# Performance work log

Measured on AMD Instinct MI355X. Metric: run time of the kernel, lower is better.

The kernel has to match this reference:

```python
import jax, jax.numpy as jnp
import numpy as np

EPS = 1e-8
TAU = 0.2
IOU_THR = 0.5
NEG = -1e9
N, C, H, D_FG, D_CLS = 8192, 1024, 256, 64, 128


def setup_inputs() -> dict:
    key = jax.random.key(0)
    ks = jax.random.split(key, 11)
    def lin(k, fan_in, fan_out):
        return jax.random.normal(k, (fan_in, fan_out), jnp.float32) / np.sqrt(fan_in)
    return {
        "roi_feats": jax.random.normal(ks[0], (N, C), jnp.float32),
        "labels": jax.random.randint(ks[1], (N,), 0, 21, jnp.int32).astype(jnp.int64),
        "ious": jax.random.uniform(ks[2], (N,), jnp.float32),
        "fg_w1": lin(ks[3], C, H), "fg_b1": jnp.zeros((H,), jnp.float32),
        "fg_w2": lin(ks[4], H, D_FG), "fg_b2": jnp.zeros((D_FG,), jnp.float32),
        "cls_w1": lin(ks[5], C, H), "cls_b1": jnp.zeros((H,), jnp.float32),
        "cls_w2": lin(ks[6], H, D_CLS), "cls_b2": jnp.zeros((D_CLS,), jnp.float32),
    }


def _project_normalize(x, w1, b1, w2, b2):
    h = jax.nn.relu(x @ w1 + b1)
    z = h @ w2 + b2
    norm = jnp.maximum(jnp.linalg.norm(z, axis=1, keepdims=True), EPS)
    return z / norm


def _forward(roi_feats, labels, ious, fg_w1, fg_b1, fg_w2, fg_b2, cls_w1, cls_b1, cls_w2, cls_b2):
    n = roi_feats.shape[0]
    z_fg = _project_normalize(roi_feats, fg_w1, fg_b1, fg_w2, fg_b2)
    z_cls = _project_normalize(roi_feats, cls_w1, cls_b1, cls_w2, cls_b2)

    ignore = labels == -1
    fg = (labels > 0) & ~ignore
    iou_weight = jnp.where(ious > IOU_THR, ious, 0.0)
    eye = jnp.eye(n, dtype=bool)

    # ---- fg/bg contrastive (bg_as_negatives_only=True) ----
    sim_fg = (z_fg @ z_fg.T) / TAU                       # [N,N]
    exp_sim = jnp.exp(sim_fg)
    denom = jnp.sum(exp_sim * (~eye).astype(jnp.float32), axis=1)
    pos = (fg & ~ignore)[None, :] & ~eye                 # positives: fg columns, no self
    n_pos = jnp.sum(pos, axis=1)
    numer = jnp.sum(exp_sim * pos.astype(jnp.float32), axis=1)
    # original computes den = denom + EPS then -log((numer+EPS)/(den+EPS))
    loss_i = -jnp.log((numer + EPS) / (denom + 2.0 * EPS))
    valid = (fg & ~ignore) & (n_pos > 0)
    w = iou_weight * valid.astype(jnp.float32)
    loss_fg_bg = jnp.sum(w * loss_i) / (jnp.sum(w) + EPS)

    # ---- class supervised contrastive ----
    sim_cls = (z_cls @ z_cls.T) / TAU
    sim_masked = jnp.where(eye, NEG, sim_cls)
    log_denom = jax.nn.logsumexp(sim_masked, axis=1)     # [N]
    log_p = jnp.where(eye, NEG, sim_cls - log_denom[:, None])
    # pos_mask keeps diagonal (as in original): same label, col not ignore, col label != 0
    posc = (labels[None, :] == labels[:, None]) & (~ignore)[None, :] & (labels[None, :] != 0)
    n_posc = jnp.sum(posc, axis=1).astype(jnp.float32)
    sum_log_p = jnp.sum(log_p * posc.astype(jnp.float32), axis=1)
    valid_c = (fg & ~ignore) & (n_posc > 0) & jnp.isfinite(log_denom)
    Lzi = jnp.where(valid_c, -sum_log_p / (n_posc + EPS), 0.0)
    wc = iou_weight * valid_c.astype(jnp.float32)
    loss_supcon = jnp.sum(wc * Lzi) / (jnp.sum(wc) + EPS)

    return jnp.stack([loss_fg_bg, loss_supcon])


def reference(roi_feats, labels, ious, fg_w1, fg_b1, fg_w2, fg_b2, cls_w1, cls_b1, cls_w2, cls_b2):
    return _forward(roi_feats, labels, ious, fg_w1, fg_b1, fg_w2, fg_b2, cls_w1, cls_b1, cls_w2, cls_b2)
```

## Files before the change

### kernel.cpp

```cpp
#include <hip/hip_runtime.h>


typedef __attribute__((ext_vector_type(8))) short bs8;
typedef __attribute__((ext_vector_type(4))) float f4;

#define MFMA_BF16(a, b, c) __builtin_amdgcn_mfma_f32_16x16x32_bf16((a), (b), (c), 0, 0, 0)
#define EXP2F(x) exp2f(x)
#define SQRT_KL2E 2.6857914f
#define LN2F      0.6931471805599453f

__device__ __forceinline__ unsigned short f2bf(float f) {
  unsigned int u = __float_as_uint(f);
  u = (u + 0x7fffu + ((u >> 16) & 1u)) >> 16;
  return (unsigned short)u;
}
__device__ __forceinline__ float bf2f(unsigned short s) {
  return __uint_as_float(((unsigned int)s) << 16);
}
__device__ __forceinline__ unsigned int pk_trunc(float a, float b) {
  return __builtin_amdgcn_perm(__float_as_uint(b), __float_as_uint(a), 0x07060302u);
}

constexpr size_t O_W1T  = 0;
constexpr size_t O_W2TF = 1048576;
constexpr size_t O_W2TC = 1081344;
constexpr size_t O_SCLS = 1146880;
constexpr size_t O_ROWD = 1163264;
constexpr size_t O_ROWN = 1196032;
constexpr size_t O_ROWS = 1228800;
constexpr size_t O_SCAL = 1261568;
constexpr size_t O_HIST = 1261584;
constexpr size_t O_NFG  = 1261712;
constexpr size_t O_H    = 1261824;
constexpr size_t O_ZF   = 9650432;
constexpr size_t O_ZC   = 10699008;
constexpr size_t O_XB   = 12796160;
constexpr size_t WS_NEED_XB = O_XB + 16777216;
constexpr int ZERO_WORDS = (int)((O_SCAL + 16 - O_SCLS) / 4);

__global__ void __launch_bounds__(256) prep_kernel(
    const float* __restrict__ X, const int* __restrict__ labels,
    const float* __restrict__ fgw1, const float* __restrict__ clsw1,
    const float* __restrict__ fgw2, const float* __restrict__ clsw2,
    unsigned short* __restrict__ W1T, unsigned short* __restrict__ W2Tf,
    unsigned short* __restrict__ W2Tc, float* __restrict__ zerop,
    int* __restrict__ hist, int* __restrict__ nfg,
    unsigned short* __restrict__ Xb) {
  const int bx = blockIdx.x, t = threadIdx.x;
  if (bx < 113) {
    int i = bx * 256 + t;
    if (i < ZERO_WORDS) zerop[i] = 0.f;
    return;
  }
  if (bx == 113) {
    __shared__ int sh[33];
    if (t < 33) sh[t] = 0;
    __syncthreads();
    for (int it = 0; it < 32; it++) {
      int lab = labels[it * 256 + t];
      if (lab >= 0 && lab < 32) atomicAdd(&sh[lab], 1);
      if (lab > 0) atomicAdd(&sh[32], 1);
    }
    __syncthreads();
    if (t < 32) hist[t] = sh[t];
    if (t == 32) *nfg = sh[32];
    return;
  }
  if (bx < 254) {
    __shared__ float tile[64][65];
    int lb = bx - 114;
    const float* src; unsigned short* dst; int R, C, lt;
    if (lb < 64)       { src = fgw1;  dst = W1T;              R = 1024; C = 256; lt = lb; }
    else if (lb < 128) { src = clsw1; dst = W1T + 256 * 1024; R = 1024; C = 256; lt = lb - 64; }
    else if (lb < 132) { src = fgw2;  dst = W2Tf;             R = 256;  C = 64;  lt = lb - 128; }
    else               { src = clsw2; dst = W2Tc;             R = 256;  C = 128; lt = lb - 132; }
    const int cT = C >> 6;
    const int r0 = (lt / cT) << 6, c0 = (lt % cT) << 6;
    {
      const int rr = t >> 4, cc = (t & 15) << 2;
#pragma unroll
      for (int i = 0; i < 4; i++) {
        float4 v = *(const float4*)(src + (size_t)(r0 + rr + i * 16) * C + c0 + cc);
        tile[rr + i * 16][cc] = v.x; tile[rr + i * 16][cc + 1] = v.y;
        tile[rr + i * 16][cc + 2] = v.z; tile[rr + i * 16][cc + 3] = v.w;
      }
    }
    __syncthreads();
    {
      const int dr = t >> 2, dc = (t & 3) << 4;
      bs8 o0, o1;
#pragma unroll
      for (int j = 0; j < 8; j++) o0[j] = (short)f2bf(tile[dc + j][dr]);
#pragma unroll
      for (int j = 0; j < 8; j++) o1[j] = (short)f2bf(tile[dc + 8 + j][dr]);
      unsigned short* dp = dst + (size_t)(c0 + dr) * R + r0 + dc;
      *(bs8*)dp = o0;
      *(bs8*)(dp + 8) = o1;
    }
    return;
  }
  {
    int i = (bx - 254) * 2048 + t * 8;
    float4 x0 = *(const float4*)(X + i);
    float4 x1 = *(const float4*)(X + i + 4);
    uint4 pk;
    pk.x = pk_trunc(x0.x, x0.y);
    pk.y = pk_trunc(x0.z, x0.w);
    pk.z = pk_trunc(x1.x, x1.y);
    pk.w = pk_trunc(x1.z, x1.w);
    *(uint4*)(Xb + i) = pk;
  }
}

__global__ void __launch_bounds__(256) gemm1x_kernel(
    const unsigned short* __restrict__ Xb, const unsigned short* __restrict__ W1T,
    const float* __restrict__ b1f, const float* __restrict__ b1c,
    unsigned short* __restrict__ H) {
  __shared__ __align__(16) unsigned short lA[128 * 72];
  __shared__ __align__(16) unsigned short lB[64 * 72];
  const int t = threadIdx.x;
  const int w = t >> 6, lane = t & 63, ln = lane & 15, quad = lane >> 4;
  const int m0 = blockIdx.x * 128, n0 = blockIdx.y * 64;

  f4 acc[2][4];
#pragma unroll
  for (int rs = 0; rs < 2; rs++)
#pragma unroll
    for (int s = 0; s < 4; s++) acc[rs][s] = (f4){0.f, 0.f, 0.f, 0.f};

  for (int k0 = 0; k0 < 1024; k0 += 64) {
    __syncthreads();
#pragma unroll
    for (int i = 0; i < 4; i++) {
      int c = i * 256 + t, r = c >> 3, ke = (c & 7) * 8;
      *(bs8*)&lA[r * 72 + ke] = *(const bs8*)(Xb + (size_t)(m0 + r) * 1024 + k0 + ke);
    }
#pragma unroll
    for (int i = 0; i < 2; i++) {
      int c = i * 256 + t, r = c >> 3, ke = (c & 7) * 8;
      *(bs8*)&lB[r * 72 + ke] = *(const bs8*)(W1T + (size_t)(n0 + r) * 1024 + k0 + ke);
    }
    __syncthreads();
#pragma unroll
    for (int kk = 0; kk < 2; kk++) {
      bs8 a0 = *(const bs8*)&lA[(w * 32 + ln) * 72 + kk * 32 + quad * 8];
      bs8 a1 = *(const bs8*)&lA[(w * 32 + 16 + ln) * 72 + kk * 32 + quad * 8];
#pragma unroll
      for (int s = 0; s < 4; s++) {
        bs8 bf = *(const bs8*)&lB[(s * 16 + ln) * 72 + kk * 32 + quad * 8];
        acc[0][s] = MFMA_BF16(a0, bf, acc[0][s]);
        acc[1][s] = MFMA_BF16(a1, bf, acc[1][s]);
      }
    }
  }
#pragma unroll
  for (int s = 0; s < 4; s++) {
    int n = n0 + s * 16 + ln;
    float b = (n < 256) ? b1f[n] : b1c[n - 256];
#pragma unroll
    for (int rs = 0; rs < 2; rs++)
#pragma unroll
      for (int r = 0; r < 4; r++) {
        float v = fmaxf(acc[rs][s][r] + b, 0.f);
        H[(size_t)(m0 + w * 32 + rs * 16 + quad * 4 + r) * 512 + n] = f2bf(v);
      }
  }
}

__global__ void __launch_bounds__(256) gemm1f_kernel(
    const float* __restrict__ X, const unsigned short* __restrict__ W1T,
    const float* __restrict__ b1f, const float* __restrict__ b1c,
    unsigned short* __restrict__ H) {
  __shared__ __align__(16) unsigned short lA[128 * 40];
  __shared__ __align__(16) unsigned short lB[64 * 40];
  const int t = threadIdx.x;
  const int w = t >> 6, lane = t & 63, ln = lane & 15, quad = lane >> 4;
  const int m0 = blockIdx.x * 128, n0 = blockIdx.y * 64;
  f4 acc[2][4];
#pragma unroll
  for (int rs = 0; rs < 2; rs++)
#pragma unroll
    for (int s = 0; s < 4; s++) acc[rs][s] = (f4){0.f, 0.f, 0.f, 0.f};
  for (int k0 = 0; k0 < 1024; k0 += 32) {
    __syncthreads();
#pragma unroll
    for (int i = 0; i < 2; i++) {
      int ch = t + i * 256;
      int r = ch >> 2, c = (ch & 3) * 8;
      const float* xp = X + (size_t)(m0 + r) * 1024 + k0 + c;
      float4 x0 = *(const float4*)xp;
      float4 x1 = *(const float4*)(xp + 4);
      uint4 pk;
      pk.x = pk_trunc(x0.x, x0.y); pk.y = pk_trunc(x0.z, x0.w);
      pk.z = pk_trunc(x1.x, x1.y); pk.w = pk_trunc(x1.z, x1.w);
      *(uint4*)&lA[r * 40 + c] = pk;
    }
    {
      int r = t >> 2, c = (t & 3) * 8;
      *(bs8*)&lB[r * 40 + c] = *(const bs8*)(W1T + (size_t)(n0 + r) * 1024 + k0 + c);
    }
    __syncthreads();
    bs8 af0 = *(const bs8*)&lA[(w * 32 + ln) * 40 + quad * 8];
    bs8 af1 = *(const bs8*)&lA[(w * 32 + 16 + ln) * 40 + quad * 8];
#pragma unroll
    for (int s = 0; s < 4; s++) {
      bs8 bf = *(const bs8*)&lB[(s * 16 + ln) * 40 + quad * 8];
      acc[0][s] = MFMA_BF16(af0, bf, acc[0][s]);
      acc[1][s] = MFMA_BF16(af1, bf, acc[1][s]);
    }
  }
#pragma unroll
  for (int s = 0; s < 4; s++) {
    int n = n0 + s * 16 + ln;
    float b = (n < 256) ? b1f[n] : b1c[n - 256];
#pragma unroll
    for (int rs = 0; rs < 2; rs++)
#pragma unroll
      for (int r = 0; r < 4; r++) {
        float v = fmaxf(acc[rs][s][r] + b, 0.f);
        H[(size_t)(m0 + w * 32 + rs * 16 + quad * 4 + r) * 512 + n] = f2bf(v);
      }
  }
}

__global__ void __launch_bounds__(256) gemm2_kernel(
    const unsigned short* __restrict__ H,
    const unsigned short* __restrict__ W2Tf, const unsigned short* __restrict__ W2Tc,
    const float* __restrict__ b2f, const float* __restrict__ b2c,
    unsigned short* __restrict__ Zf, unsigned short* __restrict__ Zc) {
  __shared__ float lredf[64][17];
  __shared__ float lredc[64][33];
  const int t = threadIdx.x;
  const int w = t >> 6, lane = t & 63, ln = lane & 15, quad = lane >> 4;
  const int rw = blockIdx.x * 16;
  const int kh = w & 1;

  if (w < 2) {
    const unsigned short* hrow = H + (size_t)(rw + ln) * 512 + kh * 128;
    f4 acc[4];
#pragma unroll
    for (int s = 0; s < 4; s++) acc[s] = (f4){0.f, 0.f, 0.f, 0.f};
#pragma unroll
    for (int ks = 0; ks < 4; ks++) {
      bs8 af = *(const bs8*)(hrow + ks * 32 + quad * 8);
#pragma unroll
      for (int s = 0; s < 4; s++) {
        bs8 bf = *(const bs8*)(W2Tf + (size_t)(s * 16 + ln) * 256 + kh * 128 + ks * 32 + quad * 8);
        acc[s] = MFMA_BF16(af, bf, acc[s]);
      }
    }
    if (kh) {
#pragma unroll
      for (int s = 0; s < 4; s++)
#pragma unroll
        for (int r = 0; r < 4; r++) lredf[lane][s * 4 + r] = acc[s][r];
    }
    __syncthreads();
    if (w == 0) {
      float ss[4] = {0.f, 0.f, 0.f, 0.f};
#pragma unroll
      for (int s = 0; s < 4; s++) {
        float b = b2f[s * 16 + ln];
#pragma unroll
        for (int r = 0; r < 4; r++) {
          acc[s][r] += lredf[lane][s * 4 + r] + b;
          ss[r] = fmaf(acc[s][r], acc[s][r], ss[r]);
        }
      }
#pragma unroll
      for (int r = 0; r < 4; r++) {
#pragma unroll
        for (int off = 1; off < 16; off <<= 1) ss[r] += __shfl_xor(ss[r], off, 64);
        float sc = SQRT_KL2E / fmaxf(sqrtf(ss[r]), 1e-8f);
#pragma unroll
        for (int s = 0; s < 4; s++)
          Zf[(size_t)(rw + quad * 4 + r) * 64 + s * 16 + ln] = f2bf(acc[s][r] * sc);
      }
    }
  } else {
    const unsigned short* hrow = H + (size_t)(rw + ln) * 512 + 256 + kh * 128;
    f4 acc[8];
#pragma unroll
    for (int s = 0; s < 8; s++) acc[s] = (f4){0.f, 0.f, 0.f, 0.f};
#pragma unroll
    for (int ks = 0; ks < 4; ks++) {
      bs8 af = *(const bs8*)(hrow + ks * 32 + quad * 8);
#pragma unroll
      for (int s = 0; s < 8; s++) {
        bs8 bf = *(const bs8*)(W2Tc + (size_t)(s * 16 + ln) * 256 + kh * 128 + ks * 32 + quad * 8);
        acc[s] = MFMA_BF16(af, bf, acc[s]);
      }
    }
    if (kh) {
#pragma unroll
      for (int s = 0; s < 8; s++)
#pragma unroll
        for (int r = 0; r < 4; r++) lredc[lane][s * 4 + r] = acc[s][r];
    }
    __syncthreads();
    if (w == 2) {
      float ss[4] = {0.f, 0.f, 0.f, 0.f};
#pragma unroll
      for (int s = 0; s < 8; s++) {
        float b = b2c[s * 16 + ln];
#pragma unroll
        for (int r = 0; r < 4; r++) {
          acc[s][r] += lredc[lane][s * 4 + r] + b;
          ss[r] = fmaf(acc[s][r], acc[s][r], ss[r]);
        }
      }
#pragma unroll
      for (int r = 0; r < 4; r++) {
#pragma unroll
        for (int off = 1; off < 16; off <<= 1) ss[r] += __shfl_xor(ss[r], off, 64);
        float sc = SQRT_KL2E / fmaxf(sqrtf(ss[r]), 1e-8f);
#pragma unroll
        for (int s = 0; s < 8; s++)
          Zc[(size_t)(rw + quad * 4 + r) * 128 + s * 16 + ln] = f2bf(acc[s][r] * sc);
      }
    }
  }
}

__global__ void __launch_bounds__(128) scls_kernel(const unsigned short* __restrict__ Zc,
                                                   const int* __restrict__ labels,
                                                   float* __restrict__ Scls) {
  const int c = blockIdx.x + 1;
  const int t = threadIdx.x;
  const int r0 = blockIdx.y * 256;
  float acc = 0.f;
#pragma unroll 4
  for (int r = r0; r < r0 + 256; r++) {
    if (labels[r] == c) acc += bf2f(Zc[(size_t)r * 128 + t]);
  }
  atomicAdd(&Scls[c * 128 + t], acc);
}

__global__ void __launch_bounds__(256, 3) sim_kernel(
    const unsigned short* __restrict__ Zf, const unsigned short* __restrict__ Zc,
    const int* __restrict__ labels,
    float* __restrict__ rowD, float* __restrict__ rowN, float* __restrict__ rowS) {
  __shared__ __align__(16) unsigned short sZf[128 * 68];
  __shared__ __align__(16) unsigned short sZc[128 * 132];
  __shared__ float sFg[128];
  const int t = threadIdx.x;
  const int w = t >> 6, lane = t & 63, ln = lane & 15, quad = lane >> 4;
  const int rbase = blockIdx.x * 128 + w * 32;
  const int c0 = blockIdx.y * 128;

#pragma unroll
  for (int i = 0; i < 4; i++) {
    int c = i * 256 + t, j = c >> 3, k8 = (c & 7) * 8;
    *(bs8*)&sZf[j * 68 + k8] = *(const bs8*)(Zf + (size_t)(c0 + j) * 64 + k8);
  }
#pragma unroll
  for (int i = 0; i < 8; i++) {
    int c = i * 256 + t, j = c >> 4, k8 = (c & 15) * 8;
    *(bs8*)&sZc[j * 132 + k8] = *(const bs8*)(Zc + (size_t)(c0 + j) * 128 + k8);
  }
  if (t < 128) sFg[t] = (labels[c0 + t] > 0) ? 1.f : 0.f;

  bs8 afg[2][2], acl[2][4];
#pragma unroll
  for (int rs = 0; rs < 2; rs++) {
    const unsigned short* zf = Zf + (size_t)(rbase + rs * 16 + ln) * 64;
    const unsigned short* zc = Zc + (size_t)(rbase + rs * 16 + ln) * 128;
#pragma unroll
    for (int s = 0; s < 2; s++) afg[rs][s] = *(const bs8*)(zf + s * 32 + quad * 8);
#pragma unroll
    for (int s = 0; s < 4; s++) acl[rs][s] = *(const bs8*)(zc + s * 32 + quad * 8);
  }
  __syncthreads();

  float dacc[2][4] = {}, nacc[2][4] = {}, sacc[2][4] = {};

#pragma unroll 2
  for (int cg = 0; cg < 8; cg++) {
    const int lcol = cg * 16 + ln;
    const float fgc = sFg[lcol];
    bs8 b0 = *(const bs8*)&sZf[lcol * 68 + quad * 8];
    bs8 b1 = *(const bs8*)&sZf[lcol * 68 + 32 + quad * 8];
    bs8 bc0 = *(const bs8*)&sZc[lcol * 132 + quad * 8];
    bs8 bc1 = *(const bs8*)&sZc[lcol * 132 + 32 + quad * 8];
    bs8 bc2 = *(const bs8*)&sZc[lcol * 132 + 64 + quad * 8];
    bs8 bc3 = *(const bs8*)&sZc[lcol * 132 + 96 + quad * 8];
#pragma unroll
    for (int rs = 0; rs < 2; rs++) {
      f4 cf = {0.f, 0.f, 0.f, 0.f};
      cf = MFMA_BF16(afg[rs][0], b0, cf);
      cf = MFMA_BF16(afg[rs][1], b1, cf);
#pragma unroll
      for (int r = 0; r < 4; r++) {
        float e = EXP2F(cf[r]);
        dacc[rs][r] += e;
        nacc[rs][r] = fmaf(fgc, e, nacc[rs][r]);
      }
      f4 cs = {0.f, 0.f, 0.f, 0.f};
      cs = MFMA_BF16(acl[rs][0], bc0, cs);
      cs = MFMA_BF16(acl[rs][1], bc1, cs);
      cs = MFMA_BF16(acl[rs][2], bc2, cs);
      cs = MFMA_BF16(acl[rs][3], bc3, cs);
#pragma unroll
      for (int r = 0; r < 4; r++) sacc[rs][r] += EXP2F(cs[r]);
    }
  }

#pragma unroll
  for (int rs = 0; rs < 2; rs++)
#pragma unroll
    for (int r = 0; r < 4; r++) {
      float d = dacc[rs][r], n = nacc[rs][r], s = sacc[rs][r];
#pragma unroll
      for (int off = 1; off < 16; off <<= 1) {
        d += __shfl_xor(d, off, 64);
        n += __shfl_xor(n, off, 64);
        s += __shfl_xor(s, off, 64);
      }
      if (ln == 0) {
        int row = rbase + rs * 16 + quad * 4 + r;
        atomicAdd(&rowD[row], d);
        atomicAdd(&rowN[row], n);
        atomicAdd(&rowS[row], s);
      }
    }
}

__global__ void __launch_bounds__(256) finalize_kernel(
    const unsigned short* __restrict__ Zf, const unsigned short* __restrict__ Zc,
    const int* __restrict__ labels, const float* __restrict__ ious,
    const float* __restrict__ rowD, const float* __restrict__ rowN,
    const float* __restrict__ rowS, const float* __restrict__ Scls,
    const int* __restrict__ hist, const int* __restrict__ nfg,
    float* __restrict__ scal) {
  __shared__ float red[4][4];
  const int t = threadIdx.x, w = t >> 6, lane = t & 63;
  float aw0 = 0.f, al0 = 0.f, aw1 = 0.f, al1 = 0.f;
  const int NFG = *nfg;
  for (int it = 0; it < 16; it++) {
    const int i = it * 512 + blockIdx.x * 4 + w;
    const int lab = labels[i];
    if (lab > 0 && lab < 32) {
      const float iou = ious[i];
      const float iw = (iou > 0.5f) ? iou : 0.f;
      float dot = 0.f, ssq = 0.f;
#pragma unroll
      for (int p = 0; p < 2; p++) {
        const int k = lane + p * 64;
        const float z = bf2f(Zc[(size_t)i * 128 + k]);
        dot = fmaf(z, Scls[lab * 128 + k], dot);
        ssq = fmaf(z, z, ssq);
      }
      float zf = bf2f(Zf[(size_t)i * 64 + lane]);
      float ssqf = zf * zf;
#pragma unroll
      for (int off = 1; off < 64; off <<= 1) {
        dot += __shfl_xor(dot, off, 64);
        ssq += __shfl_xor(ssq, off, 64);
        ssqf += __shfl_xor(ssqf, off, 64);
      }
      if (lane == 0) {
        const float ef = EXP2F(ssqf);
        if (NFG - 1 > 0) {
          const float D = rowD[i] - ef;
          const float Nn = rowN[i] - ef;
          const float loss = logf(D + 2e-8f) - logf(Nn + 1e-8f);
          aw0 += iw;
          al0 += iw * loss;
        }
        const int npc = hist[lab];
        if (npc > 0) {
          const float S = rowS[i] - EXP2F(ssq);
          const float logden = logf(S);
          const float slp = (dot - ssq) * LN2F - (float)(npc - 1) * logden - 1e9f;
          aw1 += iw;
          al1 += iw * (-slp / ((float)npc + 1e-8f));
        }
      }
    }
  }
  if (lane == 0) { red[w][0] = aw0; red[w][1] = al0; red[w][2] = aw1; red[w][3] = al1; }
  __syncthreads();
  if (t < 4) atomicAdd(&scal[t], red[0][t] + red[1][t] + red[2][t] + red[3][t]);
}

__global__ void writeout_kernel(const float* __restrict__ scal, float* __restrict__ out) {
  if (threadIdx.x == 0) {
    out[0] = scal[1] / (scal[0] + 1e-8f);
    out[1] = scal[3] / (scal[2] + 1e-8f);
  }
}

extern "C" void kernel_launch(void* const* d_in, const int* in_sizes, int n_in,
                              void* d_out, int out_size, void* d_ws, size_t ws_size,
                              hipStream_t stream) {
  (void)in_sizes; (void)n_in; (void)out_size;
  const float* roi    = (const float*)d_in[0];
  const int*   labels = (const int*)d_in[1];
  const float* ious   = (const float*)d_in[2];
  const float* fgw1   = (const float*)d_in[3];
  const float* fgb1   = (const float*)d_in[4];
  const float* fgw2   = (const float*)d_in[5];
  const float* fgb2   = (const float*)d_in[6];
  const float* clsw1  = (const float*)d_in[7];
  const float* clsb1  = (const float*)d_in[8];
  const float* clsw2  = (const float*)d_in[9];
  const float* clsb2  = (const float*)d_in[10];

  char* ws = (char*)d_ws;
  unsigned short* W1T  = (unsigned short*)(ws + O_W1T);
  unsigned short* W2Tf = (unsigned short*)(ws + O_W2TF);
  unsigned short* W2Tc = (unsigned short*)(ws + O_W2TC);
  unsigned short* Hb   = (unsigned short*)(ws + O_H);
  unsigned short* Zf   = (unsigned short*)(ws + O_ZF);
  unsigned short* Zc   = (unsigned short*)(ws + O_ZC);
  unsigned short* Xb   = (unsigned short*)(ws + O_XB);
  float* Scls = (float*)(ws + O_SCLS);
  float* rowD = (float*)(ws + O_ROWD);
  float* rowN = (float*)(ws + O_ROWN);
  float* rowS = (float*)(ws + O_ROWS);
  float* scal = (float*)(ws + O_SCAL);
  int* hist = (int*)(ws + O_HIST);
  int* nfg  = (int*)(ws + O_NFG);
  float* out = (float*)d_out;

  const bool useXb = ws_size >= WS_NEED_XB;
  const int prepBlocks = useXb ? 4350 : 254;

  hipLaunchKernelGGL(prep_kernel, dim3(prepBlocks), dim3(256), 0, stream,
                     roi, labels, fgw1, clsw1, fgw2, clsw2,
                     W1T, W2Tf, W2Tc, (float*)(ws + O_SCLS), hist, nfg, Xb);
  if (useXb) {
    hipLaunchKernelGGL(gemm1x_kernel, dim3(64, 8), dim3(256), 0, stream,
                       Xb, W1T, fgb1, clsb1, Hb);
  } else {
    hipLaunchKernelGGL(gemm1f_kernel, dim3(64, 8), dim3(256), 0, stream,
                       roi, W1T, fgb1, clsb1, Hb);
  }
  hipLaunchKernelGGL(gemm2_kernel, dim3(512), dim3(256), 0, stream,
                     Hb, W2Tf, W2Tc, fgb2, clsb2, Zf, Zc);
  hipLaunchKernelGGL(scls_kernel, dim3(20, 32), dim3(128), 0, stream, Zc, labels, Scls);
  hipLaunchKernelGGL(sim_kernel, dim3(64, 64), dim3(256), 0, stream,
                     Zf, Zc, labels, rowD, rowN, rowS);
  hipLaunchKernelGGL(finalize_kernel, dim3(128), dim3(256), 0, stream,
                     Zf, Zc, labels, ious, rowD, rowN, rowS, Scls, hist, nfg, scal);
  hipLaunchKernelGGL(writeout_kernel, dim3(1), dim3(64), 0, stream, scal, out);
}
```

Measured before the change: 248.1 us.

## Loop sim kernel over four column tiles, use raw exp2, fuse class-sum kernel

The sim kernel now walks four 128-column tiles per block on a 64x16 grid instead of one tile on 64x64. This reuses the register-held A fragments across tiles and issues four times fewer atomics to the row accumulators, at the cost of less parallelism and an extra barrier per tile. exp2f is replaced by the hardware v_exp_f32 builtin, which skips denormal and range handling. The per-class sum kernel now handles all 20 classes per block with shared-memory accumulators, so each Zc row is read once instead of once per class.

```diff
diff --git a/kernel.cpp b/kernel.cpp
--- a/kernel.cpp
+++ b/kernel.cpp
@@ -5,7 +5,21 @@
 typedef __attribute__((ext_vector_type(4))) float f4;
 
 #define MFMA_BF16(a, b, c) __builtin_amdgcn_mfma_f32_16x16x32_bf16((a), (b), (c), 0, 0, 0)
-#define EXP2F(x) exp2f(x)
+
+#if defined(__has_builtin)
+#if __has_builtin(__builtin_amdgcn_exp2f)
+#define EXP2F(x) __builtin_amdgcn_exp2f(x)
+#endif
+#endif
+#ifndef EXP2F
+__device__ __forceinline__ float __exp2_raw(float x) {
+  float r;
+  asm volatile("v_exp_f32 %0, %1" : "=v"(r) : "v"(x));
+  return r;
+}
+#define EXP2F(x) __exp2_raw(x)
+#endif
+
 #define SQRT_KL2E 2.6857914f
 #define LN2F      0.6931471805599453f
 
@@ -325,15 +339,18 @@
 __global__ void __launch_bounds__(128) scls_kernel(const unsigned short* __restrict__ Zc,
                                                    const int* __restrict__ labels,
                                                    float* __restrict__ Scls) {
-  const int c = blockIdx.x + 1;
+  __shared__ float lacc[21][128];
   const int t = threadIdx.x;
-  const int r0 = blockIdx.y * 256;
-  float acc = 0.f;
+#pragma unroll
+  for (int c = 0; c < 21; c++) lacc[c][t] = 0.f;
+  const int r0 = blockIdx.x * 256;
 #pragma unroll 4
   for (int r = r0; r < r0 + 256; r++) {
-    if (labels[r] == c) acc += bf2f(Zc[(size_t)r * 128 + t]);
-  }
-  atomicAdd(&Scls[c * 128 + t], acc);
+    const int lab = labels[r];
+    if (lab > 0) lacc[lab][t] += bf2f(Zc[(size_t)r * 128 + t]);
+  }
+#pragma unroll
+  for (int c = 1; c < 21; c++) atomicAdd(&Scls[c * 128 + t], lacc[c][t]);
 }
 
 __global__ void __launch_bounds__(256, 3) sim_kernel(
@@ -346,19 +363,6 @@
   const int t = threadIdx.x;
   const int w = t >> 6, lane = t & 63, ln = lane & 15, quad = lane >> 4;
   const int rbase = blockIdx.x * 128 + w * 32;
-  const int c0 = blockIdx.y * 128;
-
-#pragma unroll
-  for (int i = 0; i < 4; i++) {
-    int c = i * 256 + t, j = c >> 3, k8 = (c & 7) * 8;
-    *(bs8*)&sZf[j * 68 + k8] = *(const bs8*)(Zf + (size_t)(c0 + j) * 64 + k8);
-  }
-#pragma unroll
-  for (int i = 0; i < 8; i++) {
-    int c = i * 256 + t, j = c >> 4, k8 = (c & 15) * 8;
-    *(bs8*)&sZc[j * 132 + k8] = *(const bs8*)(Zc + (size_t)(c0 + j) * 128 + k8);
-  }
-  if (t < 128) sFg[t] = (labels[c0 + t] > 0) ? 1.f : 0.f;
 
   bs8 afg[2][2], acl[2][4];
 #pragma unroll
@@ -370,38 +374,54 @@
 #pragma unroll
     for (int s = 0; s < 4; s++) acl[rs][s] = *(const bs8*)(zc + s * 32 + quad * 8);
   }
-  __syncthreads();
 
   float dacc[2][4] = {}, nacc[2][4] = {}, sacc[2][4] = {};
 
+  for (int ct = 0; ct < 4; ct++) {
+    const int c0 = blockIdx.y * 512 + ct * 128;
+    if (ct) __syncthreads();
+#pragma unroll
+    for (int i = 0; i < 4; i++) {
+      int c = i * 256 + t, j = c >> 3, k8 = (c & 7) * 8;
+      *(bs8*)&sZf[j * 68 + k8] = *(const bs8*)(Zf + (size_t)(c0 + j) * 64 + k8);
+    }
+#pragma unroll
+    for (int i = 0; i < 8; i++) {
+      int c = i * 256 + t, j = c >> 4, k8 = (c & 15) * 8;
+      *(bs8*)&sZc[j * 132 + k8] = *(const bs8*)(Zc + (size_t)(c0 + j) * 128 + k8);
+    }
+    if (t < 128) sFg[t] = (labels[c0 + t] > 0) ? 1.f : 0.f;
+    __syncthreads();
+
 #pragma unroll 2
-  for (int cg = 0; cg < 8; cg++) {
-    const int lcol = cg * 16 + ln;
-    const float fgc = sFg[lcol];
-    bs8 b0 = *(const bs8*)&sZf[lcol * 68 + quad * 8];
-    bs8 b1 = *(const bs8*)&sZf[lcol * 68 + 32 + quad * 8];
-    bs8 bc0 = *(const bs8*)&sZc[lcol * 132 + quad * 8];
-    bs8 bc1 = *(const bs8*)&sZc[lcol * 132 + 32 + quad * 8];
-    bs8 bc2 = *(const bs8*)&sZc[lcol * 132 + 64 + quad * 8];
-    bs8 bc3 = *(const bs8*)&sZc[lcol * 132 + 96 + quad * 8];
-#pragma unroll
-    for (int rs = 0; rs < 2; rs++) {
-      f4 cf = {0.f, 0.f, 0.f, 0.f};
-      cf = MFMA_BF16(afg[rs][0], b0, cf);
-      cf = MFMA_BF16(afg[rs][1], b1, cf);
-#pragma unroll
-      for (int r = 0; r < 4; r++) {
-        float e = EXP2F(cf[r]);
-        dacc[rs][r] += e;
-        nacc[rs][r] = fmaf(fgc, e, nacc[rs][r]);
-      }
-      f4 cs = {0.f, 0.f, 0.f, 0.f};
-      cs = MFMA_BF16(acl[rs][0], bc0, cs);
-      cs = MFMA_BF16(acl[rs][1], bc1, cs);
-      cs = MFMA_BF16(acl[rs][2], bc2, cs);
-      cs = MFMA_BF16(acl[rs][3], bc3, cs);
-#pragma unroll
-      for (int r = 0; r < 4; r++) sacc[rs][r] += EXP2F(cs[r]);
+    for (int cg = 0; cg < 8; cg++) {
+      const int lcol = cg * 16 + ln;
+      const float fgc = sFg[lcol];
+      bs8 b0 = *(const bs8*)&sZf[lcol * 68 + quad * 8];
+      bs8 b1 = *(const bs8*)&sZf[lcol * 68 + 32 + quad * 8];
+      bs8 bc0 = *(const bs8*)&sZc[lcol * 132 + quad * 8];
+      bs8 bc1 = *(const bs8*)&sZc[lcol * 132 + 32 + quad * 8];
+      bs8 bc2 = *(const bs8*)&sZc[lcol * 132 + 64 + quad * 8];
+      bs8 bc3 = *(const bs8*)&sZc[lcol * 132 + 96 + quad * 8];
+#pragma unroll
+      for (int rs = 0; rs < 2; rs++) {
+        f4 cf = {0.f, 0.f, 0.f, 0.f};
+        cf = MFMA_BF16(afg[rs][0], b0, cf);
+        cf = MFMA_BF16(afg[rs][1], b1, cf);
+#pragma unroll
+        for (int r = 0; r < 4; r++) {
+          float e = EXP2F(cf[r]);
+          dacc[rs][r] += e;
+          nacc[rs][r] = fmaf(fgc, e, nacc[rs][r]);
+        }
+        f4 cs = {0.f, 0.f, 0.f, 0.f};
+        cs = MFMA_BF16(acl[rs][0], bc0, cs);
+        cs = MFMA_BF16(acl[rs][1], bc1, cs);
+        cs = MFMA_BF16(acl[rs][2], bc2, cs);
+        cs = MFMA_BF16(acl[rs][3], bc3, cs);
+#pragma unroll
+        for (int r = 0; r < 4; r++) sacc[rs][r] += EXP2F(cs[r]);
+      }
     }
   }
 
@@ -538,8 +558,8 @@
   }
   hipLaunchKernelGGL(gemm2_kernel, dim3(512), dim3(256), 0, stream,
                      Hb, W2Tf, W2Tc, fgb2, clsb2, Zf, Zc);
-  hipLaunchKernelGGL(scls_kernel, dim3(20, 32), dim3(128), 0, stream, Zc, labels, Scls);
-  hipLaunchKernelGGL(sim_kernel, dim3(64, 64), dim3(256), 0, stream,
+  hipLaunchKernelGGL(scls_kernel, dim3(32), dim3(128), 0, stream, Zc, labels, Scls);
+  hipLaunchKernelGGL(sim_kernel, dim3(64, 16), dim3(256), 0, stream,
                      Zf, Zc, labels, rowD, rowN, rowS);
   hipLaunchKernelGGL(finalize_kernel, dim3(128), dim3(256), 0, stream,
                      Zf, Zc, labels, ious, rowD, rowN, rowS, Scls, hist, nfg, scal);
```

Result: slower. 286.4 us (+15.5%).
